# Kernel tuning notes

Measured on AMD Instinct MI355X. Metric: run time of the kernel, lower is better.

The kernel has to match this reference:

```python
import jax, jax.numpy as jnp
import numpy as np

EPSILON = 0.1
TAU = 1.0
NORM_EPS = 1e-12  # matches torch.nn.functional.normalize eps


def setup_inputs() -> dict:
    key = jax.random.key(0)
    k_ids, k_emb = jax.random.split(key)
    B, T, V, D = 2, 2048, 50257, 768
    input_ids = jax.random.randint(k_ids, (B, T), 0, V, dtype=jnp.int64)
    embedding_weight = jax.random.normal(k_emb, (V, D), dtype=jnp.float32)
    return {"input_ids": input_ids, "embedding_weight": embedding_weight}


def _l2_normalize(x):
    # F.normalize(p=2): x / max(||x||, eps)
    n = jnp.linalg.norm(x, axis=-1, keepdims=True)
    return x / jnp.maximum(n, NORM_EPS)


def reference(input_ids, embedding_weight):
    B, T = input_ids.shape
    V, D = embedding_weight.shape
    # embedding lookup -> (B*T, D)
    vecs = embedding_weight[input_ids].reshape(B * T, D)
    vectors_norm = _l2_normalize(vecs)
    embed_norm = _l2_normalize(embedding_weight)
    # (B*T, V) similarity, scaled by epsilon/2
    scaled_sim = (vectors_norm @ embed_norm.T) * (EPSILON / 2.0)
    # gumbel_softmax (soft, tau=1): softmax((logits + gumbel) / tau)
    gkey = jax.random.key(42)
    gumbel = jax.random.gumbel(gkey, scaled_sim.shape, dtype=scaled_sim.dtype)
    weights = jax.nn.softmax((scaled_sim + gumbel) / TAU, axis=1)
    # mix back through the (unnormalized) embedding table -> (B, T, D)
    selected = weights @ embedding_weight
    return selected.reshape(B, T, D)
```

## Files before the change

kernel.cpp:

```cpp
#include <hip/hip_runtime.h>
#include <stdint.h>

constexpr int VOC  = 50257;
constexpr int VPAD = 50304;
constexpr int DEMB = 768;
constexpr int NQ   = 4096;
constexpr float EPS_HALF = 0.05f;
constexpr float MFIX = 16.0f;

#define GUMBEL_MODE 1

typedef __attribute__((ext_vector_type(4))) short    short4_t;
typedef __attribute__((ext_vector_type(8))) short    short8_t;
typedef __attribute__((ext_vector_type(4))) float    float4_t;

__device__ __forceinline__ short f2bf(float f) {
  uint32_t u = __float_as_uint(f);
  u += 0x7FFFu + ((u >> 16) & 1u);
  return (short)(u >> 16);
}
__device__ __forceinline__ float bf2f(short b) {
  return __uint_as_float(((uint32_t)(uint16_t)b) << 16);
}

__device__ __forceinline__ void tf2x32(uint32_t x0, uint32_t x1, uint32_t &o0, uint32_t &o1) {
  const uint32_t K0 = 0u;
  const uint32_t K1 = 42u;
  const uint32_t K2 = 0x1BD11BDAu ^ K0 ^ K1;
#define TFR(a) { x0 += x1; x1 = (x1 << a) | (x1 >> (32 - a)); x1 ^= x0; }
  x0 += K0; x1 += K1;
  TFR(13) TFR(15) TFR(26) TFR(6)
  x0 += K1; x1 += K2 + 1u;
  TFR(17) TFR(29) TFR(16) TFR(24)
  x0 += K2; x1 += K0 + 2u;
  TFR(13) TFR(15) TFR(26) TFR(6)
  x0 += K0; x1 += K1 + 3u;
  TFR(17) TFR(29) TFR(16) TFR(24)
  x0 += K1; x1 += K2 + 4u;
  TFR(13) TFR(15) TFR(26) TFR(6)
  x0 += K2; x1 += K0 + 5u;
#undef TFR
  o0 = x0; o1 = x1;
}

__device__ __forceinline__ float gumbel_from_bits(uint32_t bits) {
  const float LN2 = 0.69314718055994531f;
  uint32_t n = bits >> 9;
  float t;
  if (n == 0u) {
    t = 87.3365447504f;
  } else {
    uint32_t m = 8388608u - n;
    if (m < 32768u) {
      float x = (float)m * 1.1920928955078125e-7f;
      t = x * (1.0f + x * (0.5f + x * (0.3333333333f + x * 0.25f)));
    } else {
      t = (23.0f - __log2f((float)n)) * LN2;
    }
  }
  return -(__log2f(t) * LN2);
}

__device__ __forceinline__ float gumbel_at(uint32_t e) {
#if GUMBEL_MODE == 1
  uint32_t o0, o1; tf2x32(0u, e, o0, o1);
  return gumbel_from_bits(o0 ^ o1);
#else
  const uint32_t H = 102926336u;
  uint32_t o0, o1;
  if (e < H) { tf2x32(e, e + H, o0, o1); return gumbel_from_bits(o0); }
  else       { tf2x32(e - H, e, o0, o1); return gumbel_from_bits(o1); }
#endif
}

__global__ void k_prep_e(const float* __restrict__ E, short* __restrict__ Eb,
                         float* __restrict__ rk) {
  int j = blockIdx.x;
  int t = threadIdx.x;
  __shared__ float red[4];
  float ssq = 0.f;
  if (j < VOC) {
    if (t < 192) {
      float4_t v = *(const float4_t*)(E + (size_t)j * DEMB + t * 4);
      ssq = v[0]*v[0] + v[1]*v[1] + v[2]*v[2] + v[3]*v[3];
      short4_t b; b[0]=f2bf(v[0]); b[1]=f2bf(v[1]); b[2]=f2bf(v[2]); b[3]=f2bf(v[3]);
      *(short4_t*)(Eb + (size_t)j * DEMB + t * 4) = b;
    }
  } else if (t < 192) {
    short4_t z = {0,0,0,0};
    *(short4_t*)(Eb + (size_t)j * DEMB + t * 4) = z;
  }
  for (int off = 32; off; off >>= 1) ssq += __shfl_xor(ssq, off);
  if ((t & 63) == 0) red[t >> 6] = ssq;
  __syncthreads();
  if (t == 0) {
    float s = red[0] + red[1] + red[2] + red[3];
    rk[j] = (j < VOC) ? (EPS_HALF / fmaxf(sqrtf(s), 1e-12f)) : 0.f;
  }
}

__global__ void k_prep_q(const int* __restrict__ ids, const float* __restrict__ E,
                         short* __restrict__ qn) {
  int p = blockIdx.x;
  int t = threadIdx.x;
  int id = ids[p];
  __shared__ float red[4];
  __shared__ float scale_s;
  float4_t v = {0.f, 0.f, 0.f, 0.f};
  float ssq = 0.f;
  if (t < 192) {
    v = *(const float4_t*)(E + (size_t)id * DEMB + t * 4);
    ssq = v[0]*v[0] + v[1]*v[1] + v[2]*v[2] + v[3]*v[3];
  }
  for (int off = 32; off; off >>= 1) ssq += __shfl_xor(ssq, off);
  if ((t & 63) == 0) red[t >> 6] = ssq;
  __syncthreads();
  if (t == 0) scale_s = 1.0f / fmaxf(sqrtf(red[0]+red[1]+red[2]+red[3]), 1e-12f);
  __syncthreads();
  float sc = scale_s;
  if (t < 192) {
    short4_t b; b[0]=f2bf(v[0]*sc); b[1]=f2bf(v[1]*sc); b[2]=f2bf(v[2]*sc); b[3]=f2bf(v[3]*sc);
    *(short4_t*)(qn + (size_t)p * DEMB + t * 4) = b;
  }
}

__global__ void k_transpose(const short* __restrict__ Eb, short* __restrict__ Et) {
  int lane = threadIdx.x & 63;
  int dg   = threadIdx.x >> 6;
  int key  = blockIdx.x * 64 + lane;
  int d0   = blockIdx.y * 32 + dg * 8;
  short8_t v = *(const short8_t*)(Eb + (size_t)key * DEMB + d0);
#pragma unroll
  for (int q = 0; q < 8; ++q)
    Et[(size_t)(d0 + q) * VPAD + key] = v[q];
}

__global__ void k_zero(float* __restrict__ O, float* __restrict__ lsum) {
  int idx = blockIdx.x * 256 + threadIdx.x;
  if (idx < NQ) lsum[idx] = 0.f;
  float4_t z = {0.f, 0.f, 0.f, 0.f};
  ((float4_t*)O)[idx] = z;
}

__device__ __forceinline__ int swz(int row, int byte) {
  return (row << 7) + (byte ^ ((row & 7) << 4));
}

__device__ __forceinline__ void stage_bf16(short* L, const short* __restrict__ g,
                                           int row0, int rowcap, long rowstride,
                                           long col0, int tid) {
  int row = tid >> 1;
  int ch  = (tid & 1) * 64;
  long grow = row0 + row; if (grow > rowcap) grow = rowcap;
  const short8_t* src = (const short8_t*)(g + grow * rowstride + col0 + (ch >> 1));
#pragma unroll
  for (int i = 0; i < 4; ++i) {
    short8_t v = src[i];
    *(short8_t*)(L + (swz(row, ch + i * 16) >> 1)) = v;
  }
}

__device__ __forceinline__ short8_t ldfrag(const short* L, int row, int kbyte) {
  return *(const short8_t*)(L + (swz(row, kbyte) >> 1));
}

__global__ __launch_bounds__(256) void k_gemm1(
    const short* __restrict__ qn, const short* __restrict__ Eb,
    const float* __restrict__ rk, short* __restrict__ P,
    float* __restrict__ lsum, int c0, int KC) {
  __shared__ short lA[128 * 64];
  __shared__ short lB[128 * 64];
  int tid = threadIdx.x, lane = tid & 63;
  int wv = tid >> 6, wr = wv >> 1, wc = wv & 1;
  int rowbase = blockIdx.x * 128;
  int colbase = blockIdx.y * 128;
  float4_t acc[4][4];
  float4_t zero = {0.f, 0.f, 0.f, 0.f};
#pragma unroll
  for (int mt = 0; mt < 4; ++mt)
#pragma unroll
    for (int nt = 0; nt < 4; ++nt) acc[mt][nt] = zero;

  for (int kt = 0; kt < DEMB / 64; ++kt) {
    __syncthreads();
    stage_bf16(lA, qn, rowbase,      NQ - 1,   DEMB, kt * 64, tid);
    stage_bf16(lB, Eb, c0 + colbase, VPAD - 1, DEMB, kt * 64, tid);
    __syncthreads();
#pragma unroll
    for (int ks = 0; ks < 2; ++ks) {
      int kb = ks * 64 + (lane >> 4) * 16;
      short8_t a[4], b[4];
#pragma unroll
      for (int mt = 0; mt < 4; ++mt) a[mt] = ldfrag(lA, wr * 64 + mt * 16 + (lane & 15), kb);
#pragma unroll
      for (int nt = 0; nt < 4; ++nt) b[nt] = ldfrag(lB, wc * 64 + nt * 16 + (lane & 15), kb);
#pragma unroll
      for (int mt = 0; mt < 4; ++mt)
#pragma unroll
        for (int nt = 0; nt < 4; ++nt)
          acc[mt][nt] = __builtin_amdgcn_mfma_f32_16x16x32_bf16(a[mt], b[nt], acc[mt][nt], 0, 0, 0);
    }
  }
#pragma unroll
  for (int mt = 0; mt < 4; ++mt) {
    int prow = rowbase + wr * 64 + mt * 16 + ((lane >> 4) << 2);
    float rowsum[4] = {0.f, 0.f, 0.f, 0.f};
#pragma unroll
    for (int nt = 0; nt < 4; ++nt) {
      int jc = colbase + wc * 64 + nt * 16 + (lane & 15);
      int j  = c0 + jc;
      bool ok = j < VOC;
      float rkj = ok ? rk[j] : 0.f;
#pragma unroll
      for (int r = 0; r < 4; ++r) {
        int p = prow + r;
        short pb = 0;
        if (ok) {
          float s = acc[mt][nt][r] * rkj
                  + gumbel_at((uint32_t)p * (uint32_t)VOC + (uint32_t)j) - MFIX;
          pb = f2bf(__expf(s));
          rowsum[r] += bf2f(pb);
        }
        P[(size_t)p * KC + jc] = pb;
      }
    }
#pragma unroll
    for (int r = 0; r < 4; ++r) {
      float s = rowsum[r];
      s += __shfl_xor(s, 1); s += __shfl_xor(s, 2);
      s += __shfl_xor(s, 4); s += __shfl_xor(s, 8);
      if ((lane & 15) == 0) unsafeAtomicAdd(&lsum[prow + r], s);
    }
  }
}

__global__ __launch_bounds__(256) void k_gemm2(
    const short* __restrict__ P, const short* __restrict__ Et,
    float* __restrict__ O, int c0, int KC, int kseg) {
  __shared__ short lA[128 * 64];
  __shared__ short lB[128 * 64];
  int tid = threadIdx.x, lane = tid & 63;
  int wv = tid >> 6, wr = wv >> 1, wc = wv & 1;
  int rowbase = blockIdx.x * 128;
  int colbase = blockIdx.y * 128;
  int kbase   = blockIdx.z * kseg;
  float4_t acc[4][4];
  float4_t zero = {0.f, 0.f, 0.f, 0.f};
#pragma unroll
  for (int mt = 0; mt < 4; ++mt)
#pragma unroll
    for (int nt = 0; nt < 4; ++nt) acc[mt][nt] = zero;

  for (int kt = 0; kt < kseg / 64; ++kt) {
    __syncthreads();
    stage_bf16(lA, P,  rowbase, NQ - 1,   KC,   kbase + kt * 64, tid);
    stage_bf16(lB, Et, colbase, DEMB - 1, VPAD, (long)c0 + kbase + kt * 64, tid);
    __syncthreads();
#pragma unroll
    for (int ks = 0; ks < 2; ++ks) {
      int kb = ks * 64 + (lane >> 4) * 16;
      short8_t a[4], b[4];
#pragma unroll
      for (int mt = 0; mt < 4; ++mt) a[mt] = ldfrag(lA, wr * 64 + mt * 16 + (lane & 15), kb);
#pragma unroll
      for (int nt = 0; nt < 4; ++nt) b[nt] = ldfrag(lB, wc * 64 + nt * 16 + (lane & 15), kb);
#pragma unroll
      for (int mt = 0; mt < 4; ++mt)
#pragma unroll
        for (int nt = 0; nt < 4; ++nt)
          acc[mt][nt] = __builtin_amdgcn_mfma_f32_16x16x32_bf16(a[mt], b[nt], acc[mt][nt], 0, 0, 0);
    }
  }
#pragma unroll
  for (int mt = 0; mt < 4; ++mt)
#pragma unroll
    for (int nt = 0; nt < 4; ++nt) {
      int d = colbase + wc * 64 + nt * 16 + (lane & 15);
#pragma unroll
      for (int r = 0; r < 4; ++r) {
        int p = rowbase + wr * 64 + mt * 16 + ((lane >> 4) << 2) + r;
        unsafeAtomicAdd(&O[(size_t)p * DEMB + d], acc[mt][nt][r]);
      }
    }
}

__global__ void k_finalize(const float* __restrict__ O, const float* __restrict__ lsum,
                           float* __restrict__ out) {
  int idx = blockIdx.x * 256 + threadIdx.x;
  float inv = 1.0f / lsum[idx / 192];
  float4_t v = ((const float4_t*)O)[idx];
  v[0]*=inv; v[1]*=inv; v[2]*=inv; v[3]*=inv;
  ((float4_t*)out)[idx] = v;
}

extern "C" void kernel_launch(void* const* d_in, const int* in_sizes, int n_in,
                              void* d_out, int out_size, void* d_ws, size_t ws_size,
                              hipStream_t stream) {
  (void)in_sizes; (void)n_in; (void)out_size;
  const int*   ids = (const int*)d_in[0];
  const float* E   = (const float*)d_in[1];
  float*       out = (float*)d_out;

  char* w = (char*)d_ws;
  short* Eb = (short*)w;      w += (size_t)VPAD * DEMB * 2;
  short* Et = (short*)w;      w += (size_t)DEMB * VPAD * 2;
  short* qn = (short*)w;      w += (size_t)NQ * DEMB * 2;
  float* O  = (float*)w;      w += (size_t)NQ * DEMB * 4;
  float* rk = (float*)w;      w += (size_t)VPAD * 4;
  float* lsum = (float*)w;    w += NQ * 4;
  short* P  = (short*)w;
  size_t fixed = (size_t)(w - (char*)d_ws);

  int KC = 2048;
  if      (fixed + (size_t)NQ * 8192 * 2 <= ws_size) KC = 8192;
  else if (fixed + (size_t)NQ * 4096 * 2 <= ws_size) KC = 4096;
  int chunks = (VPAD + KC - 1) / KC;

  k_zero<<<(NQ * DEMB / 4) / 256, 256, 0, stream>>>(O, lsum);
  k_prep_e<<<VPAD, 256, 0, stream>>>(E, Eb, rk);
  k_prep_q<<<NQ, 256, 0, stream>>>(ids, E, qn);
  k_transpose<<<dim3(VPAD / 64, DEMB / 32), 256, 0, stream>>>(Eb, Et);

  for (int c = 0; c < chunks; ++c) {
    int c0 = c * KC;
    int KCeff = VPAD - c0; if (KCeff > KC) KCeff = KC;
    k_gemm1<<<dim3(NQ / 128, KCeff / 128), 256, 0, stream>>>(qn, Eb, rk, P, lsum, c0, KC);
    int KS = 4;
    while (KS > 1 && (KCeff % (KS * 64)) != 0) KS >>= 1;
    k_gemm2<<<dim3(NQ / 128, DEMB / 128, KS), 256, 0, stream>>>(P, Et, O, c0, KC, KCeff / KS);
  }
  k_finalize<<<(NQ * DEMB / 4) / 256, 256, 0, stream>>>(O, lsum, out);
}
```

Before: 1.484 ms.

## Simplify Gumbel epilogue algebraically and stage GEMM tiles via direct global-to-LDS loads

```diff
diff --git a/kernel.cpp b/kernel.cpp
--- a/kernel.cpp
+++ b/kernel.cpp
@@ -6,9 +6,8 @@
 constexpr int DEMB = 768;
 constexpr int NQ   = 4096;
 constexpr float EPS_HALF = 0.05f;
-constexpr float MFIX = 16.0f;
-
-#define GUMBEL_MODE 1
+constexpr float LOG2E = 1.4426950408889634f;
+constexpr float C16   = -23.083120654223414f;
 
 typedef __attribute__((ext_vector_type(4))) short    short4_t;
 typedef __attribute__((ext_vector_type(8))) short    short8_t;
@@ -23,58 +22,44 @@
   return __uint_as_float(((uint32_t)(uint16_t)b) << 16);
 }
 
-__device__ __forceinline__ void tf2x32(uint32_t x0, uint32_t x1, uint32_t &o0, uint32_t &o1) {
-  const uint32_t K0 = 0u;
-  const uint32_t K1 = 42u;
-  const uint32_t K2 = 0x1BD11BDAu ^ K0 ^ K1;
-#define TFR(a) { x0 += x1; x1 = (x1 << a) | (x1 >> (32 - a)); x1 ^= x0; }
-  x0 += K0; x1 += K1;
-  TFR(13) TFR(15) TFR(26) TFR(6)
-  x0 += K1; x1 += K2 + 1u;
-  TFR(17) TFR(29) TFR(16) TFR(24)
-  x0 += K2; x1 += K0 + 2u;
-  TFR(13) TFR(15) TFR(26) TFR(6)
-  x0 += K0; x1 += K1 + 3u;
-  TFR(17) TFR(29) TFR(16) TFR(24)
-  x0 += K1; x1 += K2 + 4u;
-  TFR(13) TFR(15) TFR(26) TFR(6)
-  x0 += K2; x1 += K0 + 5u;
-#undef TFR
-  o0 = x0; o1 = x1;
-}
-
-__device__ __forceinline__ float gumbel_from_bits(uint32_t bits) {
-  const float LN2 = 0.69314718055994531f;
+__device__ __forceinline__ void tf4(uint32_t e0, uint32_t out[4]) {
+  const uint32_t K0 = 0u, K1 = 42u, K2 = 0x1BD11BDAu ^ 42u;
+  uint32_t x0[4], x1[4];
+#pragma unroll
+  for (int r = 0; r < 4; ++r) {
+    x0[r] = K0;
+    x1[r] = (e0 + (uint32_t)r * (uint32_t)VOC) + K1;
+  }
+#define R4(a) _Pragma("unroll") \
+  for (int r = 0; r < 4; ++r) { x0[r] += x1[r]; x1[r] = __builtin_rotateleft32(x1[r], a) ^ x0[r]; }
+#define INJ(a, b, i) _Pragma("unroll") \
+  for (int r = 0; r < 4; ++r) { x0[r] += (a); x1[r] += (b) + (uint32_t)(i); }
+  R4(13) R4(15) R4(26) R4(6)
+  INJ(K1, K2, 1)
+  R4(17) R4(29) R4(16) R4(24)
+  INJ(K2, K0, 2)
+  R4(13) R4(15) R4(26) R4(6)
+  INJ(K0, K1, 3)
+  R4(17) R4(29) R4(16) R4(24)
+  INJ(K1, K2, 4)
+  R4(13) R4(15) R4(26) R4(6)
+#pragma unroll
+  for (int r = 0; r < 4; ++r) { x0[r] += K2; x1[r] += K0 + 5u; out[r] = x0[r] ^ x1[r]; }
+#undef R4
+#undef INJ
+}
+
+__device__ __forceinline__ float neg_ln_u(uint32_t bits) {
   uint32_t n = bits >> 9;
-  float t;
-  if (n == 0u) {
-    t = 87.3365447504f;
-  } else {
-    uint32_t m = 8388608u - n;
-    if (m < 32768u) {
-      float x = (float)m * 1.1920928955078125e-7f;
-      t = x * (1.0f + x * (0.5f + x * (0.3333333333f + x * 0.25f)));
-    } else {
-      t = (23.0f - __log2f((float)n)) * LN2;
-    }
-  }
-  return -(__log2f(t) * LN2);
-}
-
-__device__ __forceinline__ float gumbel_at(uint32_t e) {
-#if GUMBEL_MODE == 1
-  uint32_t o0, o1; tf2x32(0u, e, o0, o1);
-  return gumbel_from_bits(o0 ^ o1);
-#else
-  const uint32_t H = 102926336u;
-  uint32_t o0, o1;
-  if (e < H) { tf2x32(e, e + H, o0, o1); return gumbel_from_bits(o0); }
-  else       { tf2x32(e - H, e, o0, o1); return gumbel_from_bits(o1); }
-#endif
+  uint32_t m = 8388608u - n;
+  float t_log = (23.0f - __builtin_amdgcn_logf((float)n)) * 0.69314718055994531f;
+  float x = (float)m * 1.1920928955078125e-7f;
+  float t_ser = x * fmaf(x, fmaf(x, fmaf(x, 0.25f, 0.3333333333f), 0.5f), 1.0f);
+  return (m < 32768u) ? t_ser : t_log;
 }
 
 __global__ void k_prep_e(const float* __restrict__ E, short* __restrict__ Eb,
-                         float* __restrict__ rk) {
+                         float* __restrict__ rk2) {
   int j = blockIdx.x;
   int t = threadIdx.x;
   __shared__ float red[4];
@@ -95,7 +80,7 @@
   __syncthreads();
   if (t == 0) {
     float s = red[0] + red[1] + red[2] + red[3];
-    rk[j] = (j < VOC) ? (EPS_HALF / fmaxf(sqrtf(s), 1e-12f)) : 0.f;
+    rk2[j] = (j < VOC) ? (EPS_HALF * LOG2E / fmaxf(sqrtf(s), 1e-12f)) : 0.f;
   }
 }
 
@@ -146,17 +131,19 @@
   return (row << 7) + (byte ^ ((row & 7) << 4));
 }
 
-__device__ __forceinline__ void stage_bf16(short* L, const short* __restrict__ g,
-                                           int row0, int rowcap, long rowstride,
-                                           long col0, int tid) {
-  int row = tid >> 1;
-  int ch  = (tid & 1) * 64;
-  long grow = row0 + row; if (grow > rowcap) grow = rowcap;
-  const short8_t* src = (const short8_t*)(g + grow * rowstride + col0 + (ch >> 1));
+__device__ __forceinline__ void stage_g2l(short* L, const short* __restrict__ g,
+                                          long grow0, long stride, long col0, int tid) {
+  int r7 = tid >> 3;
+  int c8 = (tid & 7) << 3;
 #pragma unroll
   for (int i = 0; i < 4; ++i) {
-    short8_t v = src[i];
-    *(short8_t*)(L + (swz(row, ch + i * 16) >> 1)) = v;
+    int  row = r7 + i * 32;
+    long cs  = (long)(c8 ^ ((row & 7) << 3));
+    const short* src = g + (grow0 + row) * stride + col0 + cs;
+    short* dst = L + row * 64 + c8;
+    __builtin_amdgcn_global_load_lds(
+        (const __attribute__((address_space(1))) void*)src,
+        (__attribute__((address_space(3))) void*)dst, 16, 0, 0);
   }
 }
 
@@ -166,7 +153,7 @@
 
 __global__ __launch_bounds__(256) void k_gemm1(
     const short* __restrict__ qn, const short* __restrict__ Eb,
-    const float* __restrict__ rk, short* __restrict__ P,
+    const float* __restrict__ rk2, short* __restrict__ P,
     float* __restrict__ lsum, int c0, int KC) {
   __shared__ short lA[128 * 64];
   __shared__ short lB[128 * 64];
@@ -183,8 +170,8 @@
 
   for (int kt = 0; kt < DEMB / 64; ++kt) {
     __syncthreads();
-    stage_bf16(lA, qn, rowbase,      NQ - 1,   DEMB, kt * 64, tid);
-    stage_bf16(lB, Eb, c0 + colbase, VPAD - 1, DEMB, kt * 64, tid);
+    stage_g2l(lA, qn, rowbase,      DEMB, kt * 64, tid);
+    stage_g2l(lB, Eb, c0 + colbase, DEMB, kt * 64, tid);
     __syncthreads();
 #pragma unroll
     for (int ks = 0; ks < 2; ++ks) {
@@ -201,27 +188,31 @@
           acc[mt][nt] = __builtin_amdgcn_mfma_f32_16x16x32_bf16(a[mt], b[nt], acc[mt][nt], 0, 0, 0);
     }
   }
+  int jcb = colbase + wc * 64 + (lane & 15);
+  float rkj[4]; bool okj[4];
+#pragma unroll
+  for (int nt = 0; nt < 4; ++nt) {
+    int j = c0 + jcb + nt * 16;
+    okj[nt] = j < VOC;
+    rkj[nt] = okj[nt] ? rk2[j] : 0.f;
+  }
 #pragma unroll
   for (int mt = 0; mt < 4; ++mt) {
     int prow = rowbase + wr * 64 + mt * 16 + ((lane >> 4) << 2);
     float rowsum[4] = {0.f, 0.f, 0.f, 0.f};
 #pragma unroll
     for (int nt = 0; nt < 4; ++nt) {
-      int jc = colbase + wc * 64 + nt * 16 + (lane & 15);
-      int j  = c0 + jc;
-      bool ok = j < VOC;
-      float rkj = ok ? rk[j] : 0.f;
+      int jc = jcb + nt * 16;
+      uint32_t bits[4];
+      tf4((uint32_t)prow * (uint32_t)VOC + (uint32_t)(c0 + jc), bits);
 #pragma unroll
       for (int r = 0; r < 4; ++r) {
-        int p = prow + r;
-        short pb = 0;
-        if (ok) {
-          float s = acc[mt][nt][r] * rkj
-                  + gumbel_at((uint32_t)p * (uint32_t)VOC + (uint32_t)j) - MFIX;
-          pb = f2bf(__expf(s));
-          rowsum[r] += bf2f(pb);
-        }
-        P[(size_t)p * KC + jc] = pb;
+        float t  = neg_ln_u(bits[r]);
+        float pe = __builtin_amdgcn_exp2f(fmaf(acc[mt][nt][r], rkj[nt], C16))
+                 * __builtin_amdgcn_rcpf(t);
+        short pb = okj[nt] ? f2bf(pe) : (short)0;
+        rowsum[r] += bf2f(pb);
+        P[(size_t)(prow + r) * KC + jc] = pb;
       }
     }
 #pragma unroll
@@ -253,8 +244,8 @@
 
   for (int kt = 0; kt < kseg / 64; ++kt) {
     __syncthreads();
-    stage_bf16(lA, P,  rowbase, NQ - 1,   KC,   kbase + kt * 64, tid);
-    stage_bf16(lB, Et, colbase, DEMB - 1, VPAD, (long)c0 + kbase + kt * 64, tid);
+    stage_g2l(lA, P,  rowbase, KC,   kbase + kt * 64, tid);
+    stage_g2l(lB, Et, colbase, VPAD, (long)c0 + kbase + kt * 64, tid);
     __syncthreads();
 #pragma unroll
     for (int ks = 0; ks < 2; ++ks) {
@@ -306,7 +297,7 @@
   short* Et = (short*)w;      w += (size_t)DEMB * VPAD * 2;
   short* qn = (short*)w;      w += (size_t)NQ * DEMB * 2;
   float* O  = (float*)w;      w += (size_t)NQ * DEMB * 4;
-  float* rk = (float*)w;      w += (size_t)VPAD * 4;
+  float* rk2 = (float*)w;     w += (size_t)VPAD * 4;
   float* lsum = (float*)w;    w += NQ * 4;
   short* P  = (short*)w;
   size_t fixed = (size_t)(w - (char*)d_ws);
@@ -317,14 +308,14 @@
   int chunks = (VPAD + KC - 1) / KC;
 
   k_zero<<<(NQ * DEMB / 4) / 256, 256, 0, stream>>>(O, lsum);
-  k_prep_e<<<VPAD, 256, 0, stream>>>(E, Eb, rk);
+  k_prep_e<<<VPAD, 256, 0, stream>>>(E, Eb, rk2);
   k_prep_q<<<NQ, 256, 0, stream>>>(ids, E, qn);
   k_transpose<<<dim3(VPAD / 64, DEMB / 32), 256, 0, stream>>>(Eb, Et);
 
   for (int c = 0; c < chunks; ++c) {
     int c0 = c * KC;
     int KCeff = VPAD - c0; if (KCeff > KC) KCeff = KC;
-    k_gemm1<<<dim3(NQ / 128, KCeff / 128), 256, 0, stream>>>(qn, Eb, rk, P, lsum, c0, KC);
+    k_gemm1<<<dim3(NQ / 128, KCeff / 128), 256, 0, stream>>>(qn, Eb, rk2, P, lsum, c0, KC);
     int KS = 4;
     while (KS > 1 && (KCeff % (KS * 64)) != 0) KS >>= 1;
     k_gemm2<<<dim3(NQ / 128, DEMB / 128, KS), 256, 0, stream>>>(P, Et, O, c0, KC, KCeff / KS);
```

Result: slower. 1.560 ms (+5.2%).
